# Optimization experiments

Measured on AMD Instinct MI355X. Metric: run time of the kernel, lower is better.

Reference implementation:

```python
import jax, jax.numpy as jnp
from jax import lax
import numpy as np

ALPHA = 1.5
N_ITER = 50  # default n_iter of entmax_bisect
NUM_HEADS = 16


def _entmax_bisect_p(X):
    """entmax-bisect over last axis (Peters et al. 2019 bisection algorithm)."""
    a = ALPHA
    inv = 1.0 / (a - 1.0)  # = 2.0 for alpha=1.5
    Xa = X * (a - 1.0)
    d = X.shape[-1]
    max_val = jnp.max(Xa, axis=-1, keepdims=True)
    tau_lo = max_val - 1.0
    tau_hi = max_val - (1.0 / d) ** (a - 1.0)
    f_lo = jnp.sum(jnp.clip(Xa - tau_lo, 0.0) ** inv, axis=-1, keepdims=True) - 1.0
    dm0 = tau_hi - tau_lo

    def body(carry, _):
        tau_lo, dm, _ = carry
        dm = dm * 0.5
        tau_m = tau_lo + dm
        p_m = jnp.clip(Xa - tau_m, 0.0) ** inv
        f_m = jnp.sum(p_m, axis=-1, keepdims=True) - 1.0
        tau_lo = jnp.where(f_m * f_lo >= 0, tau_m, tau_lo)
        return (tau_lo, dm, tau_m), None

    (tau_lo, dm, tau_m), _ = lax.scan(body, (tau_lo, dm0, tau_lo), None, length=N_ITER)
    p = jnp.clip(Xa - tau_m, 0.0) ** inv
    return p / jnp.sum(p, axis=-1, keepdims=True)  # ensure_sum_one


@jax.custom_vjp
def entmax_bisect(X):
    return _entmax_bisect_p(X)


def _entmax_fwd(X):
    p = _entmax_bisect_p(X)
    return p, p


def _entmax_bwd(p, dY):
    # exact entmax Jacobian-vector product (matches entmax package backward)
    gppr = jnp.where(p > 0, p ** (2.0 - ALPHA), 0.0)
    dX = dY * gppr
    q = jnp.sum(dX, axis=-1, keepdims=True) / jnp.sum(gppr, axis=-1, keepdims=True)
    return (dX - q * gppr,)


entmax_bisect.defvjp(_entmax_fwd, _entmax_bwd)


def setup_inputs() -> dict:
    key = jax.random.key(0)
    ks = jax.random.split(key, 9)
    B, N, C = 4, 1024, 1024
    s = 0.02
    return {
        "x": jax.random.normal(ks[0], (B, N, C), dtype=jnp.float32),
        "Wq": jax.random.normal(ks[1], (C, C), dtype=jnp.float32) * s,
        "bq": jnp.zeros((C,), dtype=jnp.float32),
        "Wk": jax.random.normal(ks[2], (C, C), dtype=jnp.float32) * s,
        "bk": jnp.zeros((C,), dtype=jnp.float32),
        "Wv": jax.random.normal(ks[3], (C, C), dtype=jnp.float32) * s,
        "bv": jnp.zeros((C,), dtype=jnp.float32),
        "Wo": jax.random.normal(ks[4], (C, C), dtype=jnp.float32) * s,
        "bo": jnp.zeros((C,), dtype=jnp.float32),
    }


def reference(x, Wq, bq, Wk, bk, Wv, bv, Wo, bo):
    B, N, C = x.shape
    H = NUM_HEADS
    Dh = C // H

    def split_heads(t):  # [B,N,C] -> [B,H,N,Dh]
        return t.reshape(B, N, H, Dh).transpose(0, 2, 1, 3)

    q = split_heads(x @ Wq + bq)
    k = split_heads(x @ Wk + bk)
    v = split_heads(x @ Wv + bv)

    scores = jnp.einsum("bhnd,bhmd->bhnm", q, k) / (float(Dh) ** 0.5)
    attn = entmax_bisect(scores)  # [B,H,N,N], sparse simplex weights
    out = jnp.einsum("bhnm,bhmd->bhnd", attn, v)
    out = out.transpose(0, 2, 1, 3).reshape(B, N, C)
    return out @ Wo + bo, attn
```

## Files before the change

### kernel.cpp

```cpp
#include <hip/hip_runtime.h>
#include <hip/hip_bf16.h>
#include <stdint.h>

#define NBAT 4
#define SEQ 1024
#define CH 1024
#define NH 16
#define DH 64
#define MTOT (NBAT*SEQ)

typedef __attribute__((ext_vector_type(8))) short bf16x8;
typedef __attribute__((ext_vector_type(4))) float f32x4;
typedef unsigned short u16;

#define FENCE() asm volatile("" ::: "memory")
#define BAR() do { FENCE(); __builtin_amdgcn_s_barrier(); FENCE(); } while (0)
#define WAIT_VM0() asm volatile("s_waitcnt vmcnt(0)" ::: "memory")
#define WAIT_VM2() asm volatile("s_waitcnt vmcnt(2)" ::: "memory")
#define WAIT_VM6() asm volatile("s_waitcnt vmcnt(6)" ::: "memory")
#define WAIT_LGKM0() asm volatile("s_waitcnt lgkmcnt(0)" ::: "memory")

__device__ __forceinline__ void g2l16(void* lds, const void* g) {
  __builtin_amdgcn_global_load_lds(
      (const __attribute__((address_space(1))) uint32_t*)g,
      (__attribute__((address_space(3))) uint32_t*)lds, 16, 0, 0);
}

__device__ __forceinline__ u16 f2bf(float f) {
  union { float f; uint32_t u; } v; v.f = f;
  uint32_t lsb = (v.u >> 16) & 1u;
  v.u += 0x7fffu + lsb;
  return (u16)(v.u >> 16);
}

__device__ __forceinline__ bf16x8 ldfrag(const u16* base, int row, int koff) {
  return *(const bf16x8*)((const char*)base + row * 128 + (koff ^ ((row & 7) << 4)));
}

__global__ __launch_bounds__(256) void cvt_x(const float* __restrict__ x,
                                             u16* __restrict__ xb) {
  int i = blockIdx.x * 256 + threadIdx.x;
  float4 v = ((const float4*)x)[i];
  ushort4 o;
  o.x = f2bf(v.x); o.y = f2bf(v.y); o.z = f2bf(v.z); o.w = f2bf(v.w);
  ((ushort4*)xb)[i] = o;
}

__global__ __launch_bounds__(256) void wt_bf16(const float* __restrict__ W,
                                               u16* __restrict__ Wt) {
  __shared__ u16 tile[64][65];
  const int bi = blockIdx.x;
  const int bj = blockIdx.y;
  const int t = threadIdx.x;
  const int c4 = (t & 15) * 4, rr = t >> 4;
#pragma unroll
  for (int p = 0; p < 4; p++) {
    int r = p * 16 + rr;
    float4 v = *(const float4*)(W + (size_t)(bj * 64 + r) * CH + bi * 64 + c4);
    tile[r][c4 + 0] = f2bf(v.x); tile[r][c4 + 1] = f2bf(v.y);
    tile[r][c4 + 2] = f2bf(v.z); tile[r][c4 + 3] = f2bf(v.w);
  }
  __syncthreads();
  const int n = t >> 2, ks = (t & 3) * 16;
  u16 tmp[16];
#pragma unroll
  for (int i = 0; i < 16; i++) tmp[i] = tile[ks + i][n];
#pragma unroll
  for (int s = 0; s < 4; s++) {
    ushort4 o; o.x = tmp[4*s]; o.y = tmp[4*s+1]; o.z = tmp[4*s+2]; o.w = tmp[4*s+3];
    *(ushort4*)(Wt + (size_t)(bi * 64 + n) * CH + bj * 64 + ks + 4 * s) = o;
  }
}

template<int MODE>
__device__ __forceinline__ void gemm_body(
    u16* As, u16* Bs,
    const u16* __restrict__ A, const u16* __restrict__ Bt,
    const float* __restrict__ bias, void* __restrict__ outp,
    float scale, int bn0, int bm0, int t)
{
  const int wid = t >> 6, lane = t & 63;
  const int wr = wid >> 1, wc = wid & 1;
  const int cl = lane & 15, g = lane >> 4;

  f32x4 acc[4][4] = {};
  const u16* ga = A  + (size_t)(bm0 + (t >> 2)) * CH + (t & 3) * 8;
  const u16* gb = Bt + (size_t)(bn0 + (t >> 2)) * CH + (t & 3) * 8;

  for (int k0 = 0; k0 < CH; k0 += 32) {
    g2l16(As + t * 8,        ga + k0);
    g2l16(As + 2048 + t * 8, ga + (size_t)64 * CH + k0);
    g2l16(Bs + t * 8,        gb + k0);
    g2l16(Bs + 2048 + t * 8, gb + (size_t)64 * CH + k0);
    __syncthreads();
    bf16x8 af[4], bfr[4];
#pragma unroll
    for (int f = 0; f < 4; f++) {
      af[f]  = *(const bf16x8*)(As + (wr * 64 + f * 16 + cl) * 32 + g * 8);
      bfr[f] = *(const bf16x8*)(Bs + (wc * 64 + f * 16 + cl) * 32 + g * 8);
    }
#pragma unroll
    for (int i = 0; i < 4; i++)
#pragma unroll
      for (int j = 0; j < 4; j++)
        acc[i][j] = __builtin_amdgcn_mfma_f32_16x16x32_bf16(af[i], bfr[j], acc[i][j], 0, 0, 0);
    __syncthreads();
  }

#pragma unroll
  for (int i = 0; i < 4; i++)
#pragma unroll
    for (int j = 0; j < 4; j++) {
      const int row0 = bm0 + wr * 64 + i * 16 + g * 4;
      const int col  = bn0 + wc * 64 + j * 16 + cl;
      const float bb = bias[col];
      f32x4 v = acc[i][j];
      if (MODE == 0) {
        u16* o = (u16*)outp;
#pragma unroll
        for (int q = 0; q < 4; q++) o[(size_t)(row0 + q) * CH + col] = f2bf((v[q] + bb) * scale);
      } else if (MODE == 1) {
        u16* o = (u16*)outp;
        ushort4 pk;
        pk.x = f2bf(v[0] + bb); pk.y = f2bf(v[1] + bb);
        pk.z = f2bf(v[2] + bb); pk.w = f2bf(v[3] + bb);
        *(ushort4*)(o + (size_t)col * MTOT + row0) = pk;
      } else {
        float* o = (float*)outp;
#pragma unroll
        for (int q = 0; q < 4; q++) o[(size_t)(row0 + q) * CH + col] = v[q] + bb;
      }
    }
}

__global__ __launch_bounds__(256) void gemm_qkv(
    const u16* __restrict__ A,
    const u16* __restrict__ Wtq, const float* __restrict__ bq, u16* __restrict__ qo,
    const u16* __restrict__ Wtk, const float* __restrict__ bk, u16* __restrict__ ko,
    const u16* __restrict__ Wtv, const float* __restrict__ bv, u16* __restrict__ vo)
{
  __shared__ u16 As[128 * 32];
  __shared__ u16 Bs[128 * 32];
  const int t = threadIdx.x;
  const int bn0 = blockIdx.x * 128, bm0 = blockIdx.y * 128;
  if (blockIdx.z == 0)
    gemm_body<0>(As, Bs, A, Wtq, bq, qo, 0.0625f, bn0, bm0, t);
  else if (blockIdx.z == 1)
    gemm_body<0>(As, Bs, A, Wtk, bk, ko, 1.0f, bn0, bm0, t);
  else
    gemm_body<1>(As, Bs, A, Wtv, bv, vo, 1.0f, bn0, bm0, t);
}

__global__ __launch_bounds__(256) void gemm_out(
    const u16* __restrict__ A, const u16* __restrict__ Bt,
    const float* __restrict__ bias, float* __restrict__ outp)
{
  __shared__ u16 As[128 * 32];
  __shared__ u16 Bs[128 * 32];
  gemm_body<2>(As, Bs, A, Bt, bias, outp, 1.0f, blockIdx.x * 128, blockIdx.y * 128,
               threadIdx.x);
}

__global__ __launch_bounds__(256, 5) void fused_attn(
    const u16* __restrict__ q, const u16* __restrict__ k,
    const u16* __restrict__ vt, float* __restrict__ attn,
    u16* __restrict__ o)
{
  __shared__ u16 buf[3][64 * 64];
  __shared__ u16 pcb[4 * 256];

  const int t = threadIdx.x;
  const int w = t >> 6, lane = t & 63;
  const int cl = lane & 15, g = lane >> 4;

  const int lin = blockIdx.x;
  const int u = lin >> 3;
  const int n0 = (u & 63) * 16;
  const int bh = (lin & 7) | ((u >> 6) << 3);
  const int b = bh >> 4, h = bh & 15;
  const int r0 = w * 4;

  const u16* qb = q  + ((size_t)(b * SEQ + n0) * CH + h * DH);
  const u16* kb = k  + ((size_t)(b * SEQ) * CH + h * DH);
  const u16* vb = vt + ((size_t)(h * DH) * MTOT + b * SEQ);

  const bf16x8 aq0 = *(const bf16x8*)(qb + (size_t)(r0 + (cl & 3)) * CH + g * 8);
  const bf16x8 aq1 = *(const bf16x8*)(qb + (size_t)(r0 + (cl & 3)) * CH + 32 + g * 8);

  const int srow = t >> 3;
  const int sbyte = ((t & 7) * 16) ^ ((srow & 7) << 4);
  const int scol = sbyte >> 1;

  g2l16(buf[0] + t * 8,        kb + (size_t)srow * CH + scol);
  g2l16(buf[0] + 2048 + t * 8, kb + (size_t)(srow + 32) * CH + scol);
  g2l16(buf[1] + t * 8,        kb + (size_t)(64 + srow) * CH + scol);
  g2l16(buf[1] + 2048 + t * 8, kb + (size_t)(64 + srow + 32) * CH + scol);

  float xa[4][16];

#pragma unroll
  for (int c = 0; c < 16; ++c) {
    WAIT_LGKM0();
    if (c < 15) { WAIT_VM2(); } else { WAIT_VM0(); }
    BAR();
    if (c + 2 < 16) {
      const u16* kc = kb + (size_t)(64 * (c + 2)) * CH;
      u16* d = buf[(c + 2) % 3];
      g2l16(d + t * 8,        kc + (size_t)srow * CH + scol);
      g2l16(d + 2048 + t * 8, kc + (size_t)(srow + 32) * CH + scol);
    }
    const u16* kc = buf[c % 3];
    f32x4 sc0 = {}, sc1 = {}, sc2 = {}, sc3 = {};
    sc0 = __builtin_amdgcn_mfma_f32_16x16x32_bf16(aq0, ldfrag(kc, cl,      g * 16), sc0, 0, 0, 0);
    sc0 = __builtin_amdgcn_mfma_f32_16x16x32_bf16(aq1, ldfrag(kc, cl,      64 + g * 16), sc0, 0, 0, 0);
    sc1 = __builtin_amdgcn_mfma_f32_16x16x32_bf16(aq0, ldfrag(kc, 16 + cl, g * 16), sc1, 0, 0, 0);
    sc1 = __builtin_amdgcn_mfma_f32_16x16x32_bf16(aq1, ldfrag(kc, 16 + cl, 64 + g * 16), sc1, 0, 0, 0);
    sc2 = __builtin_amdgcn_mfma_f32_16x16x32_bf16(aq0, ldfrag(kc, 32 + cl, g * 16), sc2, 0, 0, 0);
    sc2 = __builtin_amdgcn_mfma_f32_16x16x32_bf16(aq1, ldfrag(kc, 32 + cl, 64 + g * 16), sc2, 0, 0, 0);
    sc3 = __builtin_amdgcn_mfma_f32_16x16x32_bf16(aq0, ldfrag(kc, 48 + cl, g * 16), sc3, 0, 0, 0);
    sc3 = __builtin_amdgcn_mfma_f32_16x16x32_bf16(aq1, ldfrag(kc, 48 + cl, 64 + g * 16), sc3, 0, 0, 0);
#pragma unroll
    for (int qq = 0; qq < 4; ++qq) {
      float v = sc0[qq];
      v = (g == 1) ? sc1[qq] : v;
      v = (g == 2) ? sc2[qq] : v;
      v = (g == 3) ? sc3[qq] : v;
      xa[qq][c] = v;
    }
  }

  g2l16(buf[1] + t * 8,        vb + (size_t)srow * MTOT + scol);
  g2l16(buf[1] + 2048 + t * 8, vb + (size_t)(srow + 32) * MTOT + scol);
  g2l16(buf[2] + t * 8,        vb + (size_t)srow * MTOT + 64 + scol);
  g2l16(buf[2] + 2048 + t * 8, vb + (size_t)(srow + 32) * MTOT + 64 + scol);

  float tau[4];
#pragma unroll
  for (int r = 0; r < 4; ++r) {
    float m = xa[r][0];
#pragma unroll
    for (int j = 1; j < 16; ++j) m = fmaxf(m, xa[r][j]);
#pragma unroll
    for (int off = 1; off < 64; off <<= 1) m = fmaxf(m, __shfl_xor(m, off));
    tau[r] = m - 1.0f;
  }
  for (int it = 0; it < 7; ++it) {
    float ss[4], sd[4];
#pragma unroll
    for (int r = 0; r < 4; ++r) {
      float s2 = 0.f, s1 = 0.f;
#pragma unroll
      for (int j = 0; j < 16; ++j) {
        float d = fmaxf(xa[r][j] - tau[r], 0.f);
        s2 = fmaf(d, d, s2); s1 += d;
      }
      ss[r] = s2; sd[r] = s1;
    }
#pragma unroll
    for (int off = 1; off < 64; off <<= 1) {
#pragma unroll
      for (int r = 0; r < 4; ++r) {
        ss[r] += __shfl_xor(ss[r], off);
        sd[r] += __shfl_xor(sd[r], off);
      }
    }
#pragma unroll
    for (int r = 0; r < 4; ++r)
      tau[r] += (ss[r] - 1.0f) / (sd[r] + sd[r]);
  }
  float inv[4];
#pragma unroll
  for (int r = 0; r < 4; ++r) {
    float s2 = 0.f;
#pragma unroll
    for (int j = 0; j < 16; ++j) { float d = fmaxf(xa[r][j] - tau[r], 0.f); s2 = fmaf(d, d, s2); }
#pragma unroll
    for (int off = 1; off < 64; off <<= 1) s2 += __shfl_xor(s2, off);
    inv[r] = 1.0f / s2;
  }

  char* pw = (char*)pcb + w * 512;
  f32x4 pva0 = {}, pva1 = {}, pva2 = {}, pva3 = {};
  float* ab = attn + (size_t)bh * SEQ * SEQ + (size_t)(n0 + r0) * SEQ;
#pragma unroll
  for (int vc = 0; vc < 16; ++vc) {
    float pval[4];
#pragma unroll
    for (int r = 0; r < 4; ++r) {
      float d = fmaxf(xa[r][vc] - tau[r], 0.f);
      pval[r] = d * d * inv[r];
      *(u16*)(pw + r * 128 + ((lane * 2) ^ (r << 4))) = f2bf(pval[r]);
    }
    WAIT_LGKM0();
    if (vc == 0) { WAIT_VM2(); } else { WAIT_VM6(); }
    BAR();
    if (vc + 2 < 16) {
      const u16* vc2 = vb + (size_t)64 * (vc + 2);
      u16* d = buf[(16 + vc + 2) % 3];
      g2l16(d + t * 8,        vc2 + (size_t)srow * MTOT + scol);
      g2l16(d + 2048 + t * 8, vc2 + (size_t)(srow + 32) * MTOT + scol);
    }
    const u16* vbu = buf[(16 + vc) % 3];
    const bf16x8 ap0 = *(const bf16x8*)(pw + (cl & 3) * 128 + ((g * 16) ^ ((cl & 3) << 4)));
    const bf16x8 ap1 = *(const bf16x8*)(pw + (cl & 3) * 128 + ((64 + g * 16) ^ ((cl & 3) << 4)));
    pva0 = __builtin_amdgcn_mfma_f32_16x16x32_bf16(ap0, ldfrag(vbu, cl,      g * 16), pva0, 0, 0, 0);
    pva0 = __builtin_amdgcn_mfma_f32_16x16x32_bf16(ap1, ldfrag(vbu, cl,      64 + g * 16), pva0, 0, 0, 0);
    pva1 = __builtin_amdgcn_mfma_f32_16x16x32_bf16(ap0, ldfrag(vbu, 16 + cl, g * 16), pva1, 0, 0, 0);
    pva1 = __builtin_amdgcn_mfma_f32_16x16x32_bf16(ap1, ldfrag(vbu, 16 + cl, 64 + g * 16), pva1, 0, 0, 0);
    pva2 = __builtin_amdgcn_mfma_f32_16x16x32_bf16(ap0, ldfrag(vbu, 32 + cl, g * 16), pva2, 0, 0, 0);
    pva2 = __builtin_amdgcn_mfma_f32_16x16x32_bf16(ap1, ldfrag(vbu, 32 + cl, 64 + g * 16), pva2, 0, 0, 0);
    pva3 = __builtin_amdgcn_mfma_f32_16x16x32_bf16(ap0, ldfrag(vbu, 48 + cl, g * 16), pva3, 0, 0, 0);
    pva3 = __builtin_amdgcn_mfma_f32_16x16x32_bf16(ap1, ldfrag(vbu, 48 + cl, 64 + g * 16), pva3, 0, 0, 0);
#pragma unroll
    for (int r = 0; r < 4; ++r)
      __builtin_nontemporal_store(pval[r], ab + (size_t)r * SEQ + vc * 64 + lane);
  }

  u16* ob = o + (size_t)(b * SEQ + n0 + r0) * CH + h * DH + lane;
#pragma unroll
  for (int qq = 0; qq < 4; ++qq) {
    float v = pva0[qq];
    v = (g == 1) ? pva1[qq] : v;
    v = (g == 2) ? pva2[qq] : v;
    v = (g == 3) ? pva3[qq] : v;
    ob[(size_t)qq * CH] = f2bf(v);
  }
}

extern "C" void kernel_launch(void* const* d_in, const int* in_sizes, int n_in,
                              void* d_out, int out_size, void* d_ws, size_t ws_size,
                              hipStream_t stream)
{
  const float* x  = (const float*)d_in[0];
  const float* Wq = (const float*)d_in[1];
  const float* bq = (const float*)d_in[2];
  const float* Wk = (const float*)d_in[3];
  const float* bk = (const float*)d_in[4];
  const float* Wv = (const float*)d_in[5];
  const float* bv = (const float*)d_in[6];
  const float* Wo = (const float*)d_in[7];
  const float* bo = (const float*)d_in[8];

  float* out0 = (float*)d_out;
  float* attn = out0 + (size_t)NBAT * SEQ * CH;

  const size_t T = (size_t)MTOT * CH;
  u16* xb  = (u16*)d_ws;
  u16* qw  = xb  + T;
  u16* kw  = qw  + T;
  u16* vtw = kw  + T;
  u16* ow  = vtw + T;
  u16* wtq = ow  + T;
  u16* wtk = wtq + (size_t)CH * CH;
  u16* wtv = wtk + (size_t)CH * CH;
  u16* wto = wtv + (size_t)CH * CH;

  cvt_x<<<T / (4 * 256), 256, 0, stream>>>(x, xb);
  wt_bf16<<<dim3(16, 16), 256, 0, stream>>>(Wq, wtq);
  wt_bf16<<<dim3(16, 16), 256, 0, stream>>>(Wk, wtk);
  wt_bf16<<<dim3(16, 16), 256, 0, stream>>>(Wv, wtv);
  wt_bf16<<<dim3(16, 16), 256, 0, stream>>>(Wo, wto);

  gemm_qkv<<<dim3(CH / 128, MTOT / 128, 3), 256, 0, stream>>>(
      xb, wtq, bq, qw, wtk, bk, kw, wtv, bv, vtw);

  fused_attn<<<4096, 256, 0, stream>>>(qw, kw, vtw, attn, ow);

  gemm_out<<<dim3(CH / 128, MTOT / 128), 256, 0, stream>>>(ow, wto, bo, out0);
}
```

Baseline: 270.3 us.

## Double-buffer 128-row K/V chunks in fused attention instead of triple-buffered 64-row chunks

Restructures the fused attention kernel's K and V staging from a 3-deep ring of 64-row tiles to a 2-deep ring of 128-row tiles. Each pipeline step now handles two sub-tiles, halving the number of barriers and waits in both the QK and PV loops. Probability staging grows to two LDS slots, and the wait counts change to match (vmcnt(0) in the K loop, vmcnt(8) in the V loop). The cost is less prefetch depth, since the K loop now fully drains loads every step, plus more LDS per block, with the occupancy hint lowered from 5 to 4 blocks.

Measured after the change: 245.6 us, median of 3. 1.1x faster.

```diff
diff --git a/kernel.cpp b/kernel.cpp
--- a/kernel.cpp
+++ b/kernel.cpp
@@ -16,8 +16,7 @@
 #define FENCE() asm volatile("" ::: "memory")
 #define BAR() do { FENCE(); __builtin_amdgcn_s_barrier(); FENCE(); } while (0)
 #define WAIT_VM0() asm volatile("s_waitcnt vmcnt(0)" ::: "memory")
-#define WAIT_VM2() asm volatile("s_waitcnt vmcnt(2)" ::: "memory")
-#define WAIT_VM6() asm volatile("s_waitcnt vmcnt(6)" ::: "memory")
+#define WAIT_VM8() asm volatile("s_waitcnt vmcnt(8)" ::: "memory")
 #define WAIT_LGKM0() asm volatile("s_waitcnt lgkmcnt(0)" ::: "memory")
 
 __device__ __forceinline__ void g2l16(void* lds, const void* g) {
@@ -161,13 +160,13 @@
                threadIdx.x);
 }
 
-__global__ __launch_bounds__(256, 5) void fused_attn(
+__global__ __launch_bounds__(256, 4) void fused_attn(
     const u16* __restrict__ q, const u16* __restrict__ k,
     const u16* __restrict__ vt, float* __restrict__ attn,
     u16* __restrict__ o)
 {
-  __shared__ u16 buf[3][64 * 64];
-  __shared__ u16 pcb[4 * 256];
+  __shared__ u16 buf[2][128 * 64];
+  __shared__ u16 pcb[2][4 * 256];
 
   const int t = threadIdx.x;
   const int w = t >> 6, lane = t & 63;
@@ -191,48 +190,59 @@
   const int sbyte = ((t & 7) * 16) ^ ((srow & 7) << 4);
   const int scol = sbyte >> 1;
 
-  g2l16(buf[0] + t * 8,        kb + (size_t)srow * CH + scol);
-  g2l16(buf[0] + 2048 + t * 8, kb + (size_t)(srow + 32) * CH + scol);
-  g2l16(buf[1] + t * 8,        kb + (size_t)(64 + srow) * CH + scol);
-  g2l16(buf[1] + 2048 + t * 8, kb + (size_t)(64 + srow + 32) * CH + scol);
+  {
+    u16* d = buf[0];
+    g2l16(d + t * 8,        kb + (size_t)srow * CH + scol);
+    g2l16(d + 2048 + t * 8, kb + (size_t)(srow + 32) * CH + scol);
+    g2l16(d + 4096 + t * 8, kb + (size_t)(srow + 64) * CH + scol);
+    g2l16(d + 6144 + t * 8, kb + (size_t)(srow + 96) * CH + scol);
+  }
 
   float xa[4][16];
 
 #pragma unroll
-  for (int c = 0; c < 16; ++c) {
+  for (int c = 0; c < 8; ++c) {
     WAIT_LGKM0();
-    if (c < 15) { WAIT_VM2(); } else { WAIT_VM0(); }
+    WAIT_VM0();
     BAR();
-    if (c + 2 < 16) {
-      const u16* kc = kb + (size_t)(64 * (c + 2)) * CH;
-      u16* d = buf[(c + 2) % 3];
+    if (c < 7) {
+      const u16* kc = kb + (size_t)(128 * (c + 1)) * CH;
+      u16* d = buf[(c + 1) & 1];
       g2l16(d + t * 8,        kc + (size_t)srow * CH + scol);
       g2l16(d + 2048 + t * 8, kc + (size_t)(srow + 32) * CH + scol);
-    }
-    const u16* kc = buf[c % 3];
-    f32x4 sc0 = {}, sc1 = {}, sc2 = {}, sc3 = {};
-    sc0 = __builtin_amdgcn_mfma_f32_16x16x32_bf16(aq0, ldfrag(kc, cl,      g * 16), sc0, 0, 0, 0);
-    sc0 = __builtin_amdgcn_mfma_f32_16x16x32_bf16(aq1, ldfrag(kc, cl,      64 + g * 16), sc0, 0, 0, 0);
-    sc1 = __builtin_amdgcn_mfma_f32_16x16x32_bf16(aq0, ldfrag(kc, 16 + cl, g * 16), sc1, 0, 0, 0);
-    sc1 = __builtin_amdgcn_mfma_f32_16x16x32_bf16(aq1, ldfrag(kc, 16 + cl, 64 + g * 16), sc1, 0, 0, 0);
-    sc2 = __builtin_amdgcn_mfma_f32_16x16x32_bf16(aq0, ldfrag(kc, 32 + cl, g * 16), sc2, 0, 0, 0);
-    sc2 = __builtin_amdgcn_mfma_f32_16x16x32_bf16(aq1, ldfrag(kc, 32 + cl, 64 + g * 16), sc2, 0, 0, 0);
-    sc3 = __builtin_amdgcn_mfma_f32_16x16x32_bf16(aq0, ldfrag(kc, 48 + cl, g * 16), sc3, 0, 0, 0);
-    sc3 = __builtin_amdgcn_mfma_f32_16x16x32_bf16(aq1, ldfrag(kc, 48 + cl, 64 + g * 16), sc3, 0, 0, 0);
-#pragma unroll
-    for (int qq = 0; qq < 4; ++qq) {
-      float v = sc0[qq];
-      v = (g == 1) ? sc1[qq] : v;
-      v = (g == 2) ? sc2[qq] : v;
-      v = (g == 3) ? sc3[qq] : v;
-      xa[qq][c] = v;
-    }
-  }
-
-  g2l16(buf[1] + t * 8,        vb + (size_t)srow * MTOT + scol);
-  g2l16(buf[1] + 2048 + t * 8, vb + (size_t)(srow + 32) * MTOT + scol);
-  g2l16(buf[2] + t * 8,        vb + (size_t)srow * MTOT + 64 + scol);
-  g2l16(buf[2] + 2048 + t * 8, vb + (size_t)(srow + 32) * MTOT + 64 + scol);
+      g2l16(d + 4096 + t * 8, kc + (size_t)(srow + 64) * CH + scol);
+      g2l16(d + 6144 + t * 8, kc + (size_t)(srow + 96) * CH + scol);
+    }
+#pragma unroll
+    for (int s = 0; s < 2; ++s) {
+      const u16* kc = buf[c & 1] + s * 4096;
+      f32x4 sc0 = {}, sc1 = {}, sc2 = {}, sc3 = {};
+      sc0 = __builtin_amdgcn_mfma_f32_16x16x32_bf16(aq0, ldfrag(kc, cl,      g * 16), sc0, 0, 0, 0);
+      sc0 = __builtin_amdgcn_mfma_f32_16x16x32_bf16(aq1, ldfrag(kc, cl,      64 + g * 16), sc0, 0, 0, 0);
+      sc1 = __builtin_amdgcn_mfma_f32_16x16x32_bf16(aq0, ldfrag(kc, 16 + cl, g * 16), sc1, 0, 0, 0);
+      sc1 = __builtin_amdgcn_mfma_f32_16x16x32_bf16(aq1, ldfrag(kc, 16 + cl, 64 + g * 16), sc1, 0, 0, 0);
+      sc2 = __builtin_amdgcn_mfma_f32_16x16x32_bf16(aq0, ldfrag(kc, 32 + cl, g * 16), sc2, 0, 0, 0);
+      sc2 = __builtin_amdgcn_mfma_f32_16x16x32_bf16(aq1, ldfrag(kc, 32 + cl, 64 + g * 16), sc2, 0, 0, 0);
+      sc3 = __builtin_amdgcn_mfma_f32_16x16x32_bf16(aq0, ldfrag(kc, 48 + cl, g * 16), sc3, 0, 0, 0);
+      sc3 = __builtin_amdgcn_mfma_f32_16x16x32_bf16(aq1, ldfrag(kc, 48 + cl, 64 + g * 16), sc3, 0, 0, 0);
+#pragma unroll
+      for (int qq = 0; qq < 4; ++qq) {
+        float v = sc0[qq];
+        v = (g == 1) ? sc1[qq] : v;
+        v = (g == 2) ? sc2[qq] : v;
+        v = (g == 3) ? sc3[qq] : v;
+        xa[qq][2 * c + s] = v;
+      }
+    }
+  }
+
+  {
+    u16* d = buf[0];
+    g2l16(d + t * 8,        vb + (size_t)srow * MTOT + scol);
+    g2l16(d + 2048 + t * 8, vb + (size_t)(srow + 32) * MTOT + scol);
+    g2l16(d + 4096 + t * 8, vb + (size_t)srow * MTOT + 64 + scol);
+    g2l16(d + 6144 + t * 8, vb + (size_t)(srow + 32) * MTOT + 64 + scol);
+  }
 
   float tau[4];
 #pragma unroll
@@ -279,41 +289,53 @@
     inv[r] = 1.0f / s2;
   }
 
-  char* pw = (char*)pcb + w * 512;
   f32x4 pva0 = {}, pva1 = {}, pva2 = {}, pva3 = {};
   float* ab = attn + (size_t)bh * SEQ * SEQ + (size_t)(n0 + r0) * SEQ;
 #pragma unroll
-  for (int vc = 0; vc < 16; ++vc) {
-    float pval[4];
-#pragma unroll
-    for (int r = 0; r < 4; ++r) {
-      float d = fmaxf(xa[r][vc] - tau[r], 0.f);
-      pval[r] = d * d * inv[r];
-      *(u16*)(pw + r * 128 + ((lane * 2) ^ (r << 4))) = f2bf(pval[r]);
+  for (int vc = 0; vc < 8; ++vc) {
+    float pval[2][4];
+#pragma unroll
+    for (int s = 0; s < 2; ++s) {
+      char* pw = (char*)pcb[s] + w * 512;
+#pragma unroll
+      for (int r = 0; r < 4; ++r) {
+        float d = fmaxf(xa[r][2 * vc + s] - tau[r], 0.f);
+        pval[s][r] = d * d * inv[r];
+        *(u16*)(pw + r * 128 + ((lane * 2) ^ (r << 4))) = f2bf(pval[s][r]);
+      }
     }
     WAIT_LGKM0();
-    if (vc == 0) { WAIT_VM2(); } else { WAIT_VM6(); }
+    if (vc == 0) { WAIT_VM0(); } else { WAIT_VM8(); }
     BAR();
-    if (vc + 2 < 16) {
-      const u16* vc2 = vb + (size_t)64 * (vc + 2);
-      u16* d = buf[(16 + vc + 2) % 3];
+    if (vc < 7) {
+      const u16* vc2 = vb + (size_t)128 * (vc + 1);
+      u16* d = buf[(vc + 1) & 1];
       g2l16(d + t * 8,        vc2 + (size_t)srow * MTOT + scol);
       g2l16(d + 2048 + t * 8, vc2 + (size_t)(srow + 32) * MTOT + scol);
-    }
-    const u16* vbu = buf[(16 + vc) % 3];
-    const bf16x8 ap0 = *(const bf16x8*)(pw + (cl & 3) * 128 + ((g * 16) ^ ((cl & 3) << 4)));
-    const bf16x8 ap1 = *(const bf16x8*)(pw + (cl & 3) * 128 + ((64 + g * 16) ^ ((cl & 3) << 4)));
-    pva0 = __builtin_amdgcn_mfma_f32_16x16x32_bf16(ap0, ldfrag(vbu, cl,      g * 16), pva0, 0, 0, 0);
-    pva0 = __builtin_amdgcn_mfma_f32_16x16x32_bf16(ap1, ldfrag(vbu, cl,      64 + g * 16), pva0, 0, 0, 0);
-    pva1 = __builtin_amdgcn_mfma_f32_16x16x32_bf16(ap0, ldfrag(vbu, 16 + cl, g * 16), pva1, 0, 0, 0);
-    pva1 = __builtin_amdgcn_mfma_f32_16x16x32_bf16(ap1, ldfrag(vbu, 16 + cl, 64 + g * 16), pva1, 0, 0, 0);
-    pva2 = __builtin_amdgcn_mfma_f32_16x16x32_bf16(ap0, ldfrag(vbu, 32 + cl, g * 16), pva2, 0, 0, 0);
-    pva2 = __builtin_amdgcn_mfma_f32_16x16x32_bf16(ap1, ldfrag(vbu, 32 + cl, 64 + g * 16), pva2, 0, 0, 0);
-    pva3 = __builtin_amdgcn_mfma_f32_16x16x32_bf16(ap0, ldfrag(vbu, 48 + cl, g * 16), pva3, 0, 0, 0);
-    pva3 = __builtin_amdgcn_mfma_f32_16x16x32_bf16(ap1, ldfrag(vbu, 48 + cl, 64 + g * 16), pva3, 0, 0, 0);
-#pragma unroll
-    for (int r = 0; r < 4; ++r)
-      __builtin_nontemporal_store(pval[r], ab + (size_t)r * SEQ + vc * 64 + lane);
+      g2l16(d + 4096 + t * 8, vc2 + (size_t)srow * MTOT + 64 + scol);
+      g2l16(d + 6144 + t * 8, vc2 + (size_t)(srow + 32) * MTOT + 64 + scol);
+    }
+#pragma unroll
+    for (int s = 0; s < 2; ++s) {
+      const u16* vbu = buf[vc & 1] + s * 4096;
+      const char* pw = (const char*)pcb[s] + w * 512;
+      const bf16x8 ap0 = *(const bf16x8*)(pw + (cl & 3) * 128 + ((g * 16) ^ ((cl & 3) << 4)));
+      const bf16x8 ap1 = *(const bf16x8*)(pw + (cl & 3) * 128 + ((64 + g * 16) ^ ((cl & 3) << 4)));
+      pva0 = __builtin_amdgcn_mfma_f32_16x16x32_bf16(ap0, ldfrag(vbu, cl,      g * 16), pva0, 0, 0, 0);
+      pva0 = __builtin_amdgcn_mfma_f32_16x16x32_bf16(ap1, ldfrag(vbu, cl,      64 + g * 16), pva0, 0, 0, 0);
+      pva1 = __builtin_amdgcn_mfma_f32_16x16x32_bf16(ap0, ldfrag(vbu, 16 + cl, g * 16), pva1, 0, 0, 0);
+      pva1 = __builtin_amdgcn_mfma_f32_16x16x32_bf16(ap1, ldfrag(vbu, 16 + cl, 64 + g * 16), pva1, 0, 0, 0);
+      pva2 = __builtin_amdgcn_mfma_f32_16x16x32_bf16(ap0, ldfrag(vbu, 32 + cl, g * 16), pva2, 0, 0, 0);
+      pva2 = __builtin_amdgcn_mfma_f32_16x16x32_bf16(ap1, ldfrag(vbu, 32 + cl, 64 + g * 16), pva2, 0, 0, 0);
+      pva3 = __builtin_amdgcn_mfma_f32_16x16x32_bf16(ap0, ldfrag(vbu, 48 + cl, g * 16), pva3, 0, 0, 0);
+      pva3 = __builtin_amdgcn_mfma_f32_16x16x32_bf16(ap1, ldfrag(vbu, 48 + cl, 64 + g * 16), pva3, 0, 0, 0);
+    }
+#pragma unroll
+    for (int s = 0; s < 2; ++s)
+#pragma unroll
+      for (int r = 0; r < 4; ++r)
+        __builtin_nontemporal_store(pval[s][r],
+            ab + (size_t)r * SEQ + (2 * vc + s) * 64 + lane);
   }
 
   u16* ob = o + (size_t)(b * SEQ + n0 + r0) * CH + h * DH + lane;
```

## Switch fused attention to single-wave blocks without barriers

Applied to the files above, without the earlier changes.

Restructures the fused attention kernel so each block is one 64-thread wave handling 4 query rows, and each wave streams its own K and V tiles into a private triple-buffered LDS. This removes all workgroup barriers and the inter-wave synchronisation cost. In exchange, K/V tile loads are no longer shared across waves, so global/L2 traffic for K and V quadruples. LDS use per wave also rises, which limits how many waves can be resident per CU.

Measured after the change: 399.7 us. 1.48x slower.

```diff
diff --git a/kernel.cpp b/kernel.cpp
--- a/kernel.cpp
+++ b/kernel.cpp
@@ -13,11 +13,10 @@
 typedef __attribute__((ext_vector_type(4))) float f32x4;
 typedef unsigned short u16;
 
-#define FENCE() asm volatile("" ::: "memory")
-#define BAR() do { FENCE(); __builtin_amdgcn_s_barrier(); FENCE(); } while (0)
-#define WAIT_VM0() asm volatile("s_waitcnt vmcnt(0)" ::: "memory")
-#define WAIT_VM2() asm volatile("s_waitcnt vmcnt(2)" ::: "memory")
-#define WAIT_VM6() asm volatile("s_waitcnt vmcnt(6)" ::: "memory")
+#define WAIT_VM0()  asm volatile("s_waitcnt vmcnt(0)" ::: "memory")
+#define WAIT_VM8()  asm volatile("s_waitcnt vmcnt(8)" ::: "memory")
+#define WAIT_VM12() asm volatile("s_waitcnt vmcnt(12)" ::: "memory")
+#define WAIT_VM16() asm volatile("s_waitcnt vmcnt(16)" ::: "memory")
 #define WAIT_LGKM0() asm volatile("s_waitcnt lgkmcnt(0)" ::: "memory")
 
 __device__ __forceinline__ void g2l16(void* lds, const void* g) {
@@ -161,55 +160,55 @@
                threadIdx.x);
 }
 
-__global__ __launch_bounds__(256, 5) void fused_attn(
+__global__ __launch_bounds__(64, 2) void fused_attn(
     const u16* __restrict__ q, const u16* __restrict__ k,
     const u16* __restrict__ vt, float* __restrict__ attn,
     u16* __restrict__ o)
 {
-  __shared__ u16 buf[3][64 * 64];
-  __shared__ u16 pcb[4 * 256];
-
-  const int t = threadIdx.x;
-  const int w = t >> 6, lane = t & 63;
+  __shared__ u16 kvb[3][64 * 64];
+  __shared__ u16 pcb[4 * 64];
+
+  const int lane = threadIdx.x;
   const int cl = lane & 15, g = lane >> 4;
 
   const int lin = blockIdx.x;
   const int u = lin >> 3;
-  const int n0 = (u & 63) * 16;
-  const int bh = (lin & 7) | ((u >> 6) << 3);
+  const int r0 = (u & 255) * 4;
+  const int bh = (lin & 7) | ((u >> 8) << 3);
   const int b = bh >> 4, h = bh & 15;
-  const int r0 = w * 4;
-
-  const u16* qb = q  + ((size_t)(b * SEQ + n0) * CH + h * DH);
+
+  const u16* qb = q  + ((size_t)(b * SEQ + r0) * CH + h * DH);
   const u16* kb = k  + ((size_t)(b * SEQ) * CH + h * DH);
   const u16* vb = vt + ((size_t)(h * DH) * MTOT + b * SEQ);
 
-  const bf16x8 aq0 = *(const bf16x8*)(qb + (size_t)(r0 + (cl & 3)) * CH + g * 8);
-  const bf16x8 aq1 = *(const bf16x8*)(qb + (size_t)(r0 + (cl & 3)) * CH + 32 + g * 8);
-
-  const int srow = t >> 3;
-  const int sbyte = ((t & 7) * 16) ^ ((srow & 7) << 4);
+  const bf16x8 aq0 = *(const bf16x8*)(qb + (size_t)(cl & 3) * CH + g * 8);
+  const bf16x8 aq1 = *(const bf16x8*)(qb + (size_t)(cl & 3) * CH + 32 + g * 8);
+
+  const int lrow = lane >> 3;
+  const int sbyte = ((lane & 7) * 16) ^ (lrow << 4);
   const int scol = sbyte >> 1;
 
-  g2l16(buf[0] + t * 8,        kb + (size_t)srow * CH + scol);
-  g2l16(buf[0] + 2048 + t * 8, kb + (size_t)(srow + 32) * CH + scol);
-  g2l16(buf[1] + t * 8,        kb + (size_t)(64 + srow) * CH + scol);
-  g2l16(buf[1] + 2048 + t * 8, kb + (size_t)(64 + srow + 32) * CH + scol);
+#pragma unroll
+  for (int i = 0; i < 8; ++i)
+    g2l16(kvb[0] + i * 512 + lane * 8, kb + (size_t)(8 * i + lrow) * CH + scol);
+#pragma unroll
+  for (int i = 0; i < 8; ++i)
+    g2l16(kvb[1] + i * 512 + lane * 8, kb + (size_t)(64 + 8 * i + lrow) * CH + scol);
 
   float xa[4][16];
 
 #pragma unroll
   for (int c = 0; c < 16; ++c) {
     WAIT_LGKM0();
-    if (c < 15) { WAIT_VM2(); } else { WAIT_VM0(); }
-    BAR();
+    if (c < 15) { WAIT_VM8(); } else { WAIT_VM0(); }
     if (c + 2 < 16) {
       const u16* kc = kb + (size_t)(64 * (c + 2)) * CH;
-      u16* d = buf[(c + 2) % 3];
-      g2l16(d + t * 8,        kc + (size_t)srow * CH + scol);
-      g2l16(d + 2048 + t * 8, kc + (size_t)(srow + 32) * CH + scol);
-    }
-    const u16* kc = buf[c % 3];
+      u16* d = kvb[(c + 2) % 3];
+#pragma unroll
+      for (int i = 0; i < 8; ++i)
+        g2l16(d + i * 512 + lane * 8, kc + (size_t)(8 * i + lrow) * CH + scol);
+    }
+    const u16* kc = kvb[c % 3];
     f32x4 sc0 = {}, sc1 = {}, sc2 = {}, sc3 = {};
     sc0 = __builtin_amdgcn_mfma_f32_16x16x32_bf16(aq0, ldfrag(kc, cl,      g * 16), sc0, 0, 0, 0);
     sc0 = __builtin_amdgcn_mfma_f32_16x16x32_bf16(aq1, ldfrag(kc, cl,      64 + g * 16), sc0, 0, 0, 0);
@@ -229,10 +228,13 @@
     }
   }
 
-  g2l16(buf[1] + t * 8,        vb + (size_t)srow * MTOT + scol);
-  g2l16(buf[1] + 2048 + t * 8, vb + (size_t)(srow + 32) * MTOT + scol);
-  g2l16(buf[2] + t * 8,        vb + (size_t)srow * MTOT + 64 + scol);
-  g2l16(buf[2] + 2048 + t * 8, vb + (size_t)(srow + 32) * MTOT + 64 + scol);
+  WAIT_LGKM0();
+#pragma unroll
+  for (int i = 0; i < 8; ++i)
+    g2l16(kvb[0] + i * 512 + lane * 8, vb + (size_t)(8 * i + lrow) * MTOT + scol);
+#pragma unroll
+  for (int i = 0; i < 8; ++i)
+    g2l16(kvb[1] + i * 512 + lane * 8, vb + (size_t)(8 * i + lrow) * MTOT + 64 + scol);
 
   float tau[4];
 #pragma unroll
@@ -279,9 +281,9 @@
     inv[r] = 1.0f / s2;
   }
 
-  char* pw = (char*)pcb + w * 512;
+  char* pw = (char*)pcb;
   f32x4 pva0 = {}, pva1 = {}, pva2 = {}, pva3 = {};
-  float* ab = attn + (size_t)bh * SEQ * SEQ + (size_t)(n0 + r0) * SEQ;
+  float* ab = attn + (size_t)bh * SEQ * SEQ + (size_t)r0 * SEQ;
 #pragma unroll
   for (int vc = 0; vc < 16; ++vc) {
     float pval[4];
@@ -292,15 +294,18 @@
       *(u16*)(pw + r * 128 + ((lane * 2) ^ (r << 4))) = f2bf(pval[r]);
     }
     WAIT_LGKM0();
-    if (vc == 0) { WAIT_VM2(); } else { WAIT_VM6(); }
-    BAR();
+    if (vc == 0)      { WAIT_VM8(); }
+    else if (vc == 1) { WAIT_VM12(); }
+    else if (vc < 15) { WAIT_VM16(); }
+    else              { WAIT_VM8(); }
     if (vc + 2 < 16) {
       const u16* vc2 = vb + (size_t)64 * (vc + 2);
-      u16* d = buf[(16 + vc + 2) % 3];
-      g2l16(d + t * 8,        vc2 + (size_t)srow * MTOT + scol);
-      g2l16(d + 2048 + t * 8, vc2 + (size_t)(srow + 32) * MTOT + scol);
-    }
-    const u16* vbu = buf[(16 + vc) % 3];
+      u16* d = kvb[(vc + 2) % 3];
+#pragma unroll
+      for (int i = 0; i < 8; ++i)
+        g2l16(d + i * 512 + lane * 8, vc2 + (size_t)(8 * i + lrow) * MTOT + scol);
+    }
+    const u16* vbu = kvb[vc % 3];
     const bf16x8 ap0 = *(const bf16x8*)(pw + (cl & 3) * 128 + ((g * 16) ^ ((cl & 3) << 4)));
     const bf16x8 ap1 = *(const bf16x8*)(pw + (cl & 3) * 128 + ((64 + g * 16) ^ ((cl & 3) << 4)));
     pva0 = __builtin_amdgcn_mfma_f32_16x16x32_bf16(ap0, ldfrag(vbu, cl,      g * 16), pva0, 0, 0, 0);
@@ -316,7 +321,7 @@
       __builtin_nontemporal_store(pval[r], ab + (size_t)r * SEQ + vc * 64 + lane);
   }
 
-  u16* ob = o + (size_t)(b * SEQ + n0 + r0) * CH + h * DH + lane;
+  u16* ob = o + (size_t)(b * SEQ + r0) * CH + h * DH + lane;
 #pragma unroll
   for (int qq = 0; qq < 4; ++qq) {
     float v = pva0[qq];
@@ -364,7 +369,7 @@
   gemm_qkv<<<dim3(CH / 128, MTOT / 128, 3), 256, 0, stream>>>(
       xb, wtq, bq, qw, wtk, bk, kw, wtv, bv, vtw);
 
-  fused_attn<<<4096, 256, 0, stream>>>(qw, kw, vtw, attn, ow);
+  fused_attn<<<16384, 64, 0, stream>>>(qw, kw, vtw, attn, ow);
 
   gemm_out<<<dim3(CH / 128, MTOT / 128), 256, 0, stream>>>(ow, wto, bo, out0);
 }
```
